# Kernel optimization log

Hardware: AMD Instinct MI355X
Metric: run time of the kernel (lower is better)

## Reference

```python
import jax, jax.numpy as jnp
import numpy as np

B, F, D = 4096, 32, 32
LAYER_SIZE = [128, 128]


def setup_inputs() -> dict:
    key = jax.random.key(0)
    k1, k2, k3 = jax.random.split(key, 3)
    inputs = jax.random.normal(k1, (B, F, D), dtype=jnp.float32)
    # CIN filters: shape [1, field_nums[0]*field_nums[i], field_nums[i+1]]
    field_nums = [F] + LAYER_SIZE
    filter_0 = (jax.random.normal(k2, (1, field_nums[0] * field_nums[0], field_nums[1]), dtype=jnp.float32) * 0.05)
    filter_1 = (jax.random.normal(k3, (1, field_nums[0] * field_nums[1], field_nums[2]), dtype=jnp.float32) * 0.05)
    return {"inputs": inputs, "filter_0": filter_0, "filter_1": filter_1}


def _cin_forward(inputs, filters):
    x0 = inputs          # [B, F, D] -- hidden_nn_layers[0]
    prev = inputs        # hidden_nn_layers[-1]
    outs = []
    for W in filters:    # W: [1, F*M, N]
        # outer product over field dims: [B, F, M, D]
        z = jnp.einsum('bhd,bmd->bhmd', x0, prev)
        b, h, m, d = z.shape
        z = z.reshape(b, h * m, d)                 # [B, F*M, D]
        # 1x1 conv over the F*M axis == contraction with W[0]: [F*M, N]
        cur = jnp.einsum('bpd,pn->bnd', z, W[0])   # [B, N, D]
        cur = jax.nn.relu(cur)
        prev = cur
        outs.append(cur)
    result = jnp.concatenate(outs, axis=1)         # [B, sum(layer_size), D]
    return jnp.sum(result, axis=-1)                # [B, sum(layer_size)]


def reference(inputs, filter_0, filter_1):
    return _cin_forward(inputs, (filter_0, filter_1))
```

## Files before the change

### kernel.cpp

```cpp
#include <hip/hip_runtime.h>


typedef _Float16 half_t;
typedef _Float16 half8 __attribute__((ext_vector_type(8)));
typedef float f32x4 __attribute__((ext_vector_type(4)));

template <int M>
__global__ void prep_w_kernel(const float* __restrict__ W,
                              half_t* __restrict__ Wp) {
  int gid = blockIdx.x * 256 + threadIdx.x;
  int t = gid & 31;
  int n = (gid >> 5) & 127;
  int kidx = gid >> 12;
  int h = kidx & 31;
  int mc = kidx >> 5;
  int k = h * M + mc * 32 + t;
  Wp[gid] = (half_t)W[k * 128 + n];
}

template <int M, int PSTR, bool IS_L1>
__global__ __launch_bounds__(256, 4) void cin_layer_kernel(
    const float* __restrict__ x0,
    const half_t* __restrict__ prevG,
    const half_t* __restrict__ Wp,
    half_t* __restrict__ curT,
    float* __restrict__ out,
    int outColBase) {
  __shared__ half_t xsf[4 * 32 * 32];
  __shared__ half_t prevT[4 * 32 * PSTR];

  const int tid = threadIdx.x;
  const int b0 = blockIdx.x * 4;

  const float4* x4 = (const float4*)(x0 + (size_t)b0 * 1024);
#pragma unroll
  for (int r = 0; r < 4; ++r) {
    int q = r * 256 + tid;
    float4 v = x4[q];
    int e = q * 4;
    int bi = e >> 10, h = (e >> 5) & 31, d0 = e & 31;
    half_t h0 = (half_t)v.x, h1 = (half_t)v.y, h2 = (half_t)v.z,
           h3 = (half_t)v.w;
    half_t* xp = &xsf[(bi * 32 + h) * 32 + d0];
    xp[0] = h0; xp[1] = h1; xp[2] = h2; xp[3] = h3;
    if (IS_L1) {
      prevT[(bi * 32 + d0 + 0) * PSTR + h] = h0;
      prevT[(bi * 32 + d0 + 1) * PSTR + h] = h1;
      prevT[(bi * 32 + d0 + 2) * PSTR + h] = h2;
      prevT[(bi * 32 + d0 + 3) * PSTR + h] = h3;
    }
  }
  if (!IS_L1) {
    const uint4* c4 = (const uint4*)(prevG + (size_t)b0 * 32 * 128);
#pragma unroll
    for (int r = 0; r < 8; ++r) {
      int q = r * 256 + tid;
      uint4 v = c4[q];
      int e = q * 8;
      int bi = e >> 12, d = (e >> 7) & 31, m0 = e & 127;
      *(uint4*)&prevT[(bi * 32 + d) * PSTR + m0] = v;
    }
  }
  __syncthreads();

  const int lane = tid & 63;
  const int l15 = lane & 15;
  const int quad = lane >> 4;
  const int wave = tid >> 6;
  const int wr = wave >> 1;
  const int wc = wave & 1;

  f32x4 acc[4][4];
#pragma unroll
  for (int i = 0; i < 4; ++i)
#pragma unroll
    for (int j = 0; j < 4; ++j) acc[i][j] = (f32x4){0.f, 0.f, 0.f, 0.f};

  int woff[4];
#pragma unroll
  for (int ct = 0; ct < 4; ++ct)
    woff[ct] = ((wc * 64 + ct * 16 + l15) << 5) + (quad << 3);

  constexpr int MC = M / 32;
#pragma unroll 1
  for (int mc = 0; mc < MC; ++mc) {
    half8 P[4];
#pragma unroll
    for (int rt = 0; rt < 4; ++rt) {
      int bi = wr * 2 + (rt >> 1);
      int d = (rt & 1) * 16 + l15;
      P[rt] = *(const half8*)&prevT[(bi * 32 + d) * PSTR + mc * 32 + quad * 8];
    }
#pragma unroll 2
    for (int h = 0; h < 32; ++h) {
      const half_t* wrow = Wp + (size_t)(mc * 32 + h) * 4096;
      half8 Bf[4];
#pragma unroll
      for (int ct = 0; ct < 4; ++ct)
        Bf[ct] = *(const half8*)(wrow + woff[ct]);
#pragma unroll
      for (int rt = 0; rt < 4; ++rt) {
        int bi = wr * 2 + (rt >> 1);
        int d = (rt & 1) * 16 + l15;
        half_t x = xsf[(bi * 32 + h) * 32 + d];
        half8 Af = P[rt] * x;
#pragma unroll
        for (int ct = 0; ct < 4; ++ct)
          acc[rt][ct] = __builtin_amdgcn_mfma_f32_16x16x32_f16(
              Af, Bf[ct], acc[rt][ct], 0, 0, 0);
      }
    }
  }

#pragma unroll
  for (int bil = 0; bil < 2; ++bil) {
    const int bi = wr * 2 + bil;
#pragma unroll
    for (int ct = 0; ct < 4; ++ct) {
      float s = 0.f;
#pragma unroll
      for (int dh = 0; dh < 2; ++dh) {
        const int rt = bil * 2 + dh;
        f32x4 a = acc[rt][ct];
#pragma unroll
        for (int r = 0; r < 4; ++r) {
          float v = a[r] > 0.f ? a[r] : 0.f;
          s += v;
          if (IS_L1) {
            int drow = dh * 16 + quad * 4 + r;
            curT[((size_t)(b0 + bi) * 32 + drow) * 128 + wc * 64 + ct * 16 +
                 l15] = (half_t)v;
          }
        }
      }
      s += __shfl_down(s, 32);
      s += __shfl_down(s, 16);
      if (lane < 16)
        out[(size_t)(b0 + bi) * 256 + outColBase + wc * 64 + ct * 16 + lane] =
            s;
    }
  }
}

extern "C" void kernel_launch(void* const* d_in, const int* in_sizes, int n_in,
                              void* d_out, int out_size, void* d_ws,
                              size_t ws_size, hipStream_t stream) {
  const float* x0 = (const float*)d_in[0];
  const float* w0 = (const float*)d_in[1];
  const float* w1 = (const float*)d_in[2];
  float* out = (float*)d_out;
  char* ws = (char*)d_ws;

  half_t* Wp0 = (half_t*)(ws);
  half_t* Wp1 = (half_t*)(ws + 1024 * 128 * 2);
  half_t* c1T = (half_t*)(ws + 1024 * 128 * 2 + 4096 * 128 * 2);

  hipLaunchKernelGGL((prep_w_kernel<32>), dim3(512), dim3(256), 0, stream, w0,
                     Wp0);
  hipLaunchKernelGGL((prep_w_kernel<128>), dim3(2048), dim3(256), 0, stream,
                     w1, Wp1);
  hipLaunchKernelGGL((cin_layer_kernel<32, 40, true>), dim3(1024), dim3(256),
                     0, stream, x0, (const half_t*)nullptr, Wp0, c1T, out, 0);
  hipLaunchKernelGGL((cin_layer_kernel<128, 128, false>), dim3(1024),
                     dim3(256), 0, stream, x0, c1T, Wp1, (half_t*)nullptr, out,
                     128);
}
```

Baseline: 228.5 us.

## Fuse both CIN layers into one kernel with 32x32x16 MFMA tiles

Merges the two per-layer kernels into a single kernel that keeps the first layer's ReLU output in shared memory instead of round-tripping it through a global workspace. It also switches from 16x16x32 to 32x32x16 MFMA, with each wave covering 32 output columns across all 4 batches, and repacks the weights to match the new fragment layout. This removes one launch, the global store and reload of the intermediate, and the re-staging of x0. In exchange, the first layer's shared-memory transpose buffer is reused for the intermediate, which adds barriers, and the per-wave weight load pattern changes.

```diff
diff --git a/kernel.cpp b/kernel.cpp
--- a/kernel.cpp
+++ b/kernel.cpp
@@ -2,32 +2,32 @@
 
 
 typedef _Float16 half_t;
+typedef _Float16 half4v __attribute__((ext_vector_type(4)));
 typedef _Float16 half8 __attribute__((ext_vector_type(8)));
-typedef float f32x4 __attribute__((ext_vector_type(4)));
+typedef float f32x16 __attribute__((ext_vector_type(16)));
 
 template <int M>
 __global__ void prep_w_kernel(const float* __restrict__ W,
                               half_t* __restrict__ Wp) {
   int gid = blockIdx.x * 256 + threadIdx.x;
-  int t = gid & 31;
-  int n = (gid >> 5) & 127;
-  int kidx = gid >> 12;
-  int h = kidx & 31;
-  int mc = kidx >> 5;
-  int k = h * M + mc * 32 + t;
-  Wp[gid] = (half_t)W[k * 128 + n];
+  int n = gid & 127;
+  int r = gid >> 7;
+  int t = r & 15;
+  int s = r >> 4;
+  int h = s & 31;
+  int mc = s >> 5;
+  int k = h * M + mc * 16 + t;
+  Wp[(((s * 2 + (t >> 3)) * 128 + n) << 3) + (t & 7)] = (half_t)W[k * 128 + n];
 }
 
-template <int M, int PSTR, bool IS_L1>
-__global__ __launch_bounds__(256, 4) void cin_layer_kernel(
+__global__ __launch_bounds__(256, 4) void cin_fused_kernel(
     const float* __restrict__ x0,
-    const half_t* __restrict__ prevG,
-    const half_t* __restrict__ Wp,
-    half_t* __restrict__ curT,
-    float* __restrict__ out,
-    int outColBase) {
+    const half_t* __restrict__ Wp0,
+    const half_t* __restrict__ Wp1,
+    float* __restrict__ out) {
   __shared__ half_t xsf[4 * 32 * 32];
-  __shared__ half_t prevT[4 * 32 * PSTR];
+  __shared__ half_t prevT[4 * 32 * 128];
+  half_t* xT = prevT;
 
   const int tid = threadIdx.x;
   const int b0 = blockIdx.x * 4;
@@ -39,106 +39,98 @@
     float4 v = x4[q];
     int e = q * 4;
     int bi = e >> 10, h = (e >> 5) & 31, d0 = e & 31;
-    half_t h0 = (half_t)v.x, h1 = (half_t)v.y, h2 = (half_t)v.z,
-           h3 = (half_t)v.w;
-    half_t* xp = &xsf[(bi * 32 + h) * 32 + d0];
-    xp[0] = h0; xp[1] = h1; xp[2] = h2; xp[3] = h3;
-    if (IS_L1) {
-      prevT[(bi * 32 + d0 + 0) * PSTR + h] = h0;
-      prevT[(bi * 32 + d0 + 1) * PSTR + h] = h1;
-      prevT[(bi * 32 + d0 + 2) * PSTR + h] = h2;
-      prevT[(bi * 32 + d0 + 3) * PSTR + h] = h3;
-    }
-  }
-  if (!IS_L1) {
-    const uint4* c4 = (const uint4*)(prevG + (size_t)b0 * 32 * 128);
-#pragma unroll
-    for (int r = 0; r < 8; ++r) {
-      int q = r * 256 + tid;
-      uint4 v = c4[q];
-      int e = q * 8;
-      int bi = e >> 12, d = (e >> 7) & 31, m0 = e & 127;
-      *(uint4*)&prevT[(bi * 32 + d) * PSTR + m0] = v;
-    }
+    half4v hv = {(half_t)v.x, (half_t)v.y, (half_t)v.z, (half_t)v.w};
+    *(half4v*)&xsf[(bi * 32 + h) * 32 + d0] = hv;
+    xT[(bi * 32 + d0 + 0) * 40 + h] = hv[0];
+    xT[(bi * 32 + d0 + 1) * 40 + h] = hv[1];
+    xT[(bi * 32 + d0 + 2) * 40 + h] = hv[2];
+    xT[(bi * 32 + d0 + 3) * 40 + h] = hv[3];
   }
   __syncthreads();
 
   const int lane = tid & 63;
-  const int l15 = lane & 15;
-  const int quad = lane >> 4;
+  const int l31 = lane & 31;
+  const int hi = lane >> 5;
   const int wave = tid >> 6;
-  const int wr = wave >> 1;
-  const int wc = wave & 1;
+  const int n0 = wave * 32;
 
-  f32x4 acc[4][4];
+  const f32x16 z16 = {0.f, 0.f, 0.f, 0.f, 0.f, 0.f, 0.f, 0.f,
+                      0.f, 0.f, 0.f, 0.f, 0.f, 0.f, 0.f, 0.f};
+  f32x16 acc[4];
 #pragma unroll
-  for (int i = 0; i < 4; ++i)
-#pragma unroll
-    for (int j = 0; j < 4; ++j) acc[i][j] = (f32x4){0.f, 0.f, 0.f, 0.f};
+  for (int rt = 0; rt < 4; ++rt) acc[rt] = z16;
 
-  int woff[4];
-#pragma unroll
-  for (int ct = 0; ct < 4; ++ct)
-    woff[ct] = ((wc * 64 + ct * 16 + l15) << 5) + (quad << 3);
+  const half_t* wp0 = Wp0 + (size_t)hi * 1024 + (size_t)(n0 + l31) * 8;
+  const half_t* wp1 = Wp1 + (size_t)hi * 1024 + (size_t)(n0 + l31) * 8;
 
-  constexpr int MC = M / 32;
 #pragma unroll 1
-  for (int mc = 0; mc < MC; ++mc) {
+  for (int mc = 0; mc < 2; ++mc) {
     half8 P[4];
 #pragma unroll
-    for (int rt = 0; rt < 4; ++rt) {
-      int bi = wr * 2 + (rt >> 1);
-      int d = (rt & 1) * 16 + l15;
-      P[rt] = *(const half8*)&prevT[(bi * 32 + d) * PSTR + mc * 32 + quad * 8];
-    }
+    for (int rt = 0; rt < 4; ++rt)
+      P[rt] = *(const half8*)&xT[(rt * 32 + l31) * 40 + mc * 16 + hi * 8];
+    const half_t* wrow = wp0 + (size_t)mc * 32 * 2048;
 #pragma unroll 2
     for (int h = 0; h < 32; ++h) {
-      const half_t* wrow = Wp + (size_t)(mc * 32 + h) * 4096;
-      half8 Bf[4];
-#pragma unroll
-      for (int ct = 0; ct < 4; ++ct)
-        Bf[ct] = *(const half8*)(wrow + woff[ct]);
+      half8 Bf = *(const half8*)(wrow + (size_t)h * 2048);
 #pragma unroll
       for (int rt = 0; rt < 4; ++rt) {
-        int bi = wr * 2 + (rt >> 1);
-        int d = (rt & 1) * 16 + l15;
-        half_t x = xsf[(bi * 32 + h) * 32 + d];
-        half8 Af = P[rt] * x;
+        half_t xv = xsf[(rt * 32 + h) * 32 + l31];
+        half8 Af = P[rt] * xv;
+        acc[rt] = __builtin_amdgcn_mfma_f32_32x32x16_f16(Af, Bf, acc[rt], 0, 0, 0);
+      }
+    }
+  }
+
+  __syncthreads();
+
 #pragma unroll
-        for (int ct = 0; ct < 4; ++ct)
-          acc[rt][ct] = __builtin_amdgcn_mfma_f32_16x16x32_f16(
-              Af, Bf[ct], acc[rt][ct], 0, 0, 0);
+  for (int rt = 0; rt < 4; ++rt) {
+    float s = 0.f;
+#pragma unroll
+    for (int r = 0; r < 16; ++r) {
+      float v = acc[rt][r];
+      v = v > 0.f ? v : 0.f;
+      s += v;
+      int d = (r & 3) + ((r >> 2) * 8) + hi * 4;
+      prevT[(rt * 32 + d) * 128 + n0 + l31] = (half_t)v;
+    }
+    s += __shfl_down(s, 32);
+    if (lane < 32) out[(size_t)(b0 + rt) * 256 + n0 + lane] = s;
+    acc[rt] = z16;
+  }
+  __syncthreads();
+
+#pragma unroll 1
+  for (int mc = 0; mc < 8; ++mc) {
+    half8 P[4];
+#pragma unroll
+    for (int rt = 0; rt < 4; ++rt)
+      P[rt] = *(const half8*)&prevT[(rt * 32 + l31) * 128 + mc * 16 + hi * 8];
+    const half_t* wrow = wp1 + (size_t)mc * 32 * 2048;
+#pragma unroll 2
+    for (int h = 0; h < 32; ++h) {
+      half8 Bf = *(const half8*)(wrow + (size_t)h * 2048);
+#pragma unroll
+      for (int rt = 0; rt < 4; ++rt) {
+        half_t xv = xsf[(rt * 32 + h) * 32 + l31];
+        half8 Af = P[rt] * xv;
+        acc[rt] = __builtin_amdgcn_mfma_f32_32x32x16_f16(Af, Bf, acc[rt], 0, 0, 0);
       }
     }
   }
 
 #pragma unroll
-  for (int bil = 0; bil < 2; ++bil) {
-    const int bi = wr * 2 + bil;
+  for (int rt = 0; rt < 4; ++rt) {
+    float s = 0.f;
 #pragma unroll
-    for (int ct = 0; ct < 4; ++ct) {
-      float s = 0.f;
-#pragma unroll
-      for (int dh = 0; dh < 2; ++dh) {
-        const int rt = bil * 2 + dh;
-        f32x4 a = acc[rt][ct];
-#pragma unroll
-        for (int r = 0; r < 4; ++r) {
-          float v = a[r] > 0.f ? a[r] : 0.f;
-          s += v;
-          if (IS_L1) {
-            int drow = dh * 16 + quad * 4 + r;
-            curT[((size_t)(b0 + bi) * 32 + drow) * 128 + wc * 64 + ct * 16 +
-                 l15] = (half_t)v;
-          }
-        }
-      }
-      s += __shfl_down(s, 32);
-      s += __shfl_down(s, 16);
-      if (lane < 16)
-        out[(size_t)(b0 + bi) * 256 + outColBase + wc * 64 + ct * 16 + lane] =
-            s;
+    for (int r = 0; r < 16; ++r) {
+      float v = acc[rt][r];
+      s += v > 0.f ? v : 0.f;
     }
+    s += __shfl_down(s, 32);
+    if (lane < 32)
+      out[(size_t)(b0 + rt) * 256 + 128 + n0 + lane] = s;
   }
 }
 
@@ -152,16 +144,12 @@
   char* ws = (char*)d_ws;
 
   half_t* Wp0 = (half_t*)(ws);
-  half_t* Wp1 = (half_t*)(ws + 1024 * 128 * 2);
-  half_t* c1T = (half_t*)(ws + 1024 * 128 * 2 + 4096 * 128 * 2);
+  half_t* Wp1 = (half_t*)(ws + 64 * 2048 * 2);
 
   hipLaunchKernelGGL((prep_w_kernel<32>), dim3(512), dim3(256), 0, stream, w0,
                      Wp0);
   hipLaunchKernelGGL((prep_w_kernel<128>), dim3(2048), dim3(256), 0, stream,
                      w1, Wp1);
-  hipLaunchKernelGGL((cin_layer_kernel<32, 40, true>), dim3(1024), dim3(256),
-                     0, stream, x0, (const half_t*)nullptr, Wp0, c1T, out, 0);
-  hipLaunchKernelGGL((cin_layer_kernel<128, 128, false>), dim3(1024),
-                     dim3(256), 0, stream, x0, c1T, Wp1, (half_t*)nullptr, out,
-                     128);
+  hipLaunchKernelGGL(cin_fused_kernel, dim3(1024), dim3(256), 0, stream, x0,
+                     Wp0, Wp1, out);
 }
```

Measured after the change: 217.0 us. -5.0%, faster.
